# Kernel tuning notes

Hardware: AMD Instinct MI355X
Metric: run time of the kernel (lower is better)

## Reference

```python
import jax, jax.numpy as jnp
import numpy as np

N, D, E, H, K = 4096, 512, 32, 128, 4  # tokens, d_model, n_experts, expert hidden, top-k


def setup_inputs() -> dict:
    key = jax.random.key(0)
    k0, k1, k2, k3 = jax.random.split(key, 4)
    x = jax.random.normal(k0, (N, D), dtype=jnp.float32)
    # router weights, init std = d**-0.5 (matches get_initializer std)
    expert_sel = jax.random.normal(k1, (E, D), dtype=jnp.float32) * (D ** -0.5)
    # per-expert MLP weights (Linear stores [out, in]; we keep [E, in, out] layout)
    w1 = jax.random.normal(k2, (E, D, H), dtype=jnp.float32) * (D ** -0.5)
    w2 = jax.random.normal(k3, (E, H, D), dtype=jnp.float32) * (H ** -0.5)
    return {"x": x, "expert_sel": expert_sel, "w1": w1, "w2": w2}


def reference(x, expert_sel, w1, w2):
    # routing: sigmoid selection, top-k experts per token
    scores = jax.nn.sigmoid(x @ expert_sel.T)          # [N, E]
    gate_vals, gate_idx = jax.lax.top_k(scores, K)     # [N, K]
    # dense gate matrix with only top-k nonzero (sparse dispatch/combine weights)
    gate = (jax.nn.one_hot(gate_idx, E, dtype=x.dtype) * gate_vals[..., None]).sum(-2)  # [N, E]
    # per-expert MLP; gating at hidden is exact since experts have no bias:
    # gate * (relu(x W1) W2) == (gate * relu(x W1)) W2
    h = jax.nn.relu(jnp.einsum('nd,edh->neh', x, w1)) * gate[..., None]  # [N, E, H]
    y = jnp.einsum('neh,ehv->nv', h, w2)               # [N, D]
    return y
```

## Files before the change

### kernel.cpp

```cpp
#include <hip/hip_runtime.h>
#include <hip/hip_bf16.h>

#define NTOK 4096
#define DM   512
#define NE   32
#define HD   128
#define TK   4

typedef unsigned short u16;
typedef unsigned int   u32;
typedef u16   u16x4 __attribute__((ext_vector_type(4)));
typedef u16   u16x8 __attribute__((ext_vector_type(8)));
typedef short short8 __attribute__((ext_vector_type(8)));
typedef float f32x4 __attribute__((ext_vector_type(4)));

__device__ __forceinline__ u16 f2bf(float f) {
    union { float f; u32 u; } v; v.f = f;
    return (u16)((v.u + 0x7FFFu + ((v.u >> 16) & 1u)) >> 16);
}
__device__ __forceinline__ float bf2f(u16 h) {
    union { u32 u; float f; } v; v.u = ((u32)h) << 16; return v.f;
}

__global__ __launch_bounds__(256) void prep_kernel(const float* __restrict__ x,
                                                   const float* __restrict__ sel,
                                                   const float* __restrict__ w1,
                                                   const float* __restrict__ w2,
                                                   int* __restrict__ counts_pad,
                                                   int* __restrict__ tok_list,
                                                   float* __restrict__ gate_list,
                                                   u16* __restrict__ xbf,
                                                   u16* __restrict__ wf1,
                                                   u16* __restrict__ wf2) {
    __shared__ float  xs[4][520];
    __shared__ double sc[4][33];
    int tid = threadIdx.x;
    int wv = tid >> 6, lane = tid & 63;

    if (blockIdx.x >= 1024) {
        int m = lane & 15, q = lane >> 4;
        int f0 = ((blockIdx.x - 1024) * 4 + wv) * 2;
        const float* in[2]; u16* outp[2]; int Nd[2];
#pragma unroll
        for (int u = 0; u < 2; ++u) {
            int w = f0 + u;
            if (w < 4096) {
                int e = w >> 7, rem = w & 127, ks = rem >> 3, nt = rem & 7;
                in[u] = w1 + (size_t)e * DM * HD + (size_t)(32 * ks + q * 8) * HD + 16 * nt + m;
                Nd[u] = HD;
                outp[u] = wf1 + (size_t)w * 512 + lane * 8;
            } else {
                int wl = w - 4096, e = wl >> 7, rem = wl & 127, ks = rem >> 5, nt = rem & 31;
                in[u] = w2 + (size_t)e * HD * DM + (size_t)(32 * ks + q * 8) * DM + 16 * nt + m;
                Nd[u] = DM;
                outp[u] = wf2 + (size_t)wl * 512 + lane * 8;
            }
        }
        float v[2][8];
#pragma unroll
        for (int u = 0; u < 2; ++u)
#pragma unroll
            for (int j = 0; j < 8; ++j) v[u][j] = in[u][(size_t)j * Nd[u]];
#pragma unroll
        for (int u = 0; u < 2; ++u) {
            u16x8 h;
#pragma unroll
            for (int j = 0; j < 8; ++j) h[j] = f2bf(v[u][j]);
            *(u16x8*)outp[u] = h;
        }
        return;
    }

    int tb = blockIdx.x * 4;
#pragma unroll
    for (int rep = 0; rep < 2; ++rep) {
        int idx = (rep * 256 + tid) * 4;
        int row = idx >> 9, col = idx & 511;
        f32x4 v = *(const f32x4*)(x + (size_t)(tb + row) * DM + col);
        *(f32x4*)&xs[row][col] = v;
        u16x4 h;
#pragma unroll
        for (int j = 0; j < 4; ++j) h[j] = f2bf(v[j]);
        *(u16x4*)(xbf + (size_t)(tb + row) * DM + col) = h;
    }
    __syncthreads();

    int tok = tid & 3, seg = (tid >> 2) & 1, e = tid >> 3;
    const float* sp = sel + (size_t)e * DM + seg * 256;
    const float* xp = &xs[tok][seg * 256];
    double pa = 0.0, pb = 0.0, pc = 0.0, pd = 0.0;
#pragma unroll 4
    for (int j = 0; j < 256; j += 16) {
        f32x4 x0 = *(const f32x4*)(xp + j);
        f32x4 x1 = *(const f32x4*)(xp + j + 4);
        f32x4 x2 = *(const f32x4*)(xp + j + 8);
        f32x4 x3 = *(const f32x4*)(xp + j + 12);
        f32x4 s0 = *(const f32x4*)(sp + j);
        f32x4 s1 = *(const f32x4*)(sp + j + 4);
        f32x4 s2 = *(const f32x4*)(sp + j + 8);
        f32x4 s3 = *(const f32x4*)(sp + j + 12);
#pragma unroll
        for (int k = 0; k < 4; ++k) {
            pa = fma((double)x0[k], (double)s0[k], pa);
            pb = fma((double)x1[k], (double)s1[k], pb);
            pc = fma((double)x2[k], (double)s2[k], pc);
            pd = fma((double)x3[k], (double)s3[k], pd);
        }
    }
    double p = (pa + pb) + (pc + pd);
    p += __shfl_xor(p, 4);
    if (seg == 0) sc[tok][e] = p;
    __syncthreads();

    if (tid < 4) {
        int t = tb + tid;
        unsigned mask = 0;
        for (int k = 0; k < TK; ++k) {
            double best = -1e300; int be = 0;
            for (int ee = 0; ee < NE; ++ee) {
                double v = sc[tid][ee];
                if (!((mask >> ee) & 1u) && v > best) { best = v; be = ee; }
            }
            mask |= 1u << be;
            float gate = 1.0f / (1.0f + __expf(-(float)best));
            int pos = atomicAdd(&counts_pad[32 * be], 1);
            tok_list[be * NTOK + pos]  = (k << 16) | t;
            gate_list[be * NTOK + pos] = gate;
        }
    }
}

__global__ __launch_bounds__(256, 2) void moe_mlp_kernel(const u16* __restrict__ xbf,
                                                         const u16* __restrict__ wf1,
                                                         const u16* __restrict__ wf2,
                                                         const int* __restrict__ counts_pad,
                                                         const int* __restrict__ tok_list,
                                                         const float* __restrict__ gate_list,
                                                         u16* __restrict__ part,
                                                         float* __restrict__ out,
                                                         int use_part) {
    __shared__ int   s_cnt[NE];
    __shared__ int   s_ent[32];
    __shared__ float s_gate[32];
    __shared__ __align__(16) u16 Hm[32][136];
    __shared__ __align__(16) u16 Ct[32][520];

    int tid = threadIdx.x;
    if (tid < NE) s_cnt[tid] = counts_pad[32 * tid];
    __syncthreads();

    int b = blockIdx.x;
    int xcd = b & 7, idx = b >> 3;
    int e = -1, t = 0, rows = 0, pre = 0;
#pragma unroll
    for (int j = 0; j < 4; ++j) {
        int ee = xcd + 8 * j;
        int cc = s_cnt[ee];
        int nt = (cc + 31) >> 5;
        if (e < 0 && idx < pre + nt) { e = ee; t = idx - pre; rows = cc - t * 32; if (rows > 32) rows = 32; }
        pre += nt;
    }
    if (e < 0) return;

    if (tid < 32) {
        int base = e * NTOK + t * 32;
        bool val = tid < rows;
        s_ent[tid]  = tok_list[base + (val ? tid : 0)];
        s_gate[tid] = val ? gate_list[base + tid] : 0.0f;
    }
    __syncthreads();

    int wv = tid >> 6, lane = tid & 63, m = lane & 15, q = lane >> 4;
    int r = wv >> 1, c = wv & 1;
    const u16* w1f = wf1 + (size_t)e * (128 * 512);
    const u16* w2f = wf2 + (size_t)e * (128 * 512);

    const u16* a0 = xbf + (size_t)(s_ent[16 * r + m] & 0xFFFF) * DM + q * 8;

    short8 ab[2][2];
    short8 bb[2][2][4];
#pragma unroll
    for (int kk = 0; kk < 2; ++kk) {
        ab[0][kk] = *(const short8*)(a0 + 32 * kk);
        const u16* bp = w1f + (size_t)kk * 4096 + (size_t)(4 * c) * 512 + lane * 8;
#pragma unroll
        for (int n = 0; n < 4; ++n) bb[0][kk][n] = *(const short8*)(bp + n * 512);
    }
    f32x4 acc[4];
#pragma unroll
    for (int n = 0; n < 4; ++n) acc[n] = (f32x4){0.f, 0.f, 0.f, 0.f};

#pragma unroll
    for (int kp = 0; kp < 8; ++kp) {
        int cur = kp & 1, nxt = cur ^ 1;
        if (kp < 7) {
            int ks0 = 2 * (kp + 1);
#pragma unroll
            for (int kk = 0; kk < 2; ++kk) {
                ab[nxt][kk] = *(const short8*)(a0 + 32 * (ks0 + kk));
                const u16* bp = w1f + (size_t)(ks0 + kk) * 4096 + (size_t)(4 * c) * 512 + lane * 8;
#pragma unroll
                for (int n = 0; n < 4; ++n) bb[nxt][kk][n] = *(const short8*)(bp + n * 512);
            }
        }
#pragma unroll
        for (int kk = 0; kk < 2; ++kk)
#pragma unroll
            for (int n = 0; n < 4; ++n)
                acc[n] = __builtin_amdgcn_mfma_f32_16x16x32_bf16(ab[cur][kk],
                                                                 bb[cur][kk][n],
                                                                 acc[n], 0, 0, 0);
    }

    {
        int rb = 16 * r + q * 4;
#pragma unroll
        for (int n = 0; n < 4; ++n)
#pragma unroll
            for (int rr = 0; rr < 4; ++rr)
                Hm[rb + rr][64 * c + 16 * n + m] =
                    f2bf(fmaxf(acc[n][rr], 0.f) * s_gate[rb + rr]);
    }

    short8 cb[2][8];
    {
        const u16* bp = w2f + (size_t)(wv * 8) * 512 + lane * 8;
#pragma unroll
        for (int n = 0; n < 8; ++n) cb[0][n] = *(const short8*)(bp + n * 512);
    }
    __syncthreads();

    f32x4 acc2[2][8];
#pragma unroll
    for (int i = 0; i < 2; ++i)
#pragma unroll
        for (int n = 0; n < 8; ++n) acc2[i][n] = (f32x4){0.f, 0.f, 0.f, 0.f};
#pragma unroll
    for (int ks = 0; ks < 4; ++ks) {
        int cur = ks & 1, nxt = cur ^ 1;
        if (ks < 3) {
            const u16* bp = w2f + (size_t)((ks + 1) * 32 + wv * 8) * 512 + lane * 8;
#pragma unroll
            for (int n = 0; n < 8; ++n) cb[nxt][n] = *(const short8*)(bp + n * 512);
        }
        short8 h0 = *(const short8*)&Hm[m][32 * ks + q * 8];
        short8 h1 = *(const short8*)&Hm[16 + m][32 * ks + q * 8];
#pragma unroll
        for (int n = 0; n < 8; ++n) {
            acc2[0][n] = __builtin_amdgcn_mfma_f32_16x16x32_bf16(h0, cb[cur][n], acc2[0][n], 0, 0, 0);
            acc2[1][n] = __builtin_amdgcn_mfma_f32_16x16x32_bf16(h1, cb[cur][n], acc2[1][n], 0, 0, 0);
        }
    }

#pragma unroll
    for (int i = 0; i < 2; ++i) {
        int rb = 16 * i + q * 4;
#pragma unroll
        for (int n = 0; n < 8; ++n)
#pragma unroll
            for (int rr = 0; rr < 4; ++rr)
                Ct[rb + rr][128 * wv + 16 * n + m] = f2bf(acc2[i][n][rr]);
    }
    __syncthreads();
#pragma unroll
    for (int rep = 0; rep < 8; ++rep) {
        int rl = rep * 4 + wv;
        u16x8 v = *(const u16x8*)&Ct[rl][lane * 8];
        if (rl < rows) {
            int en = s_ent[rl];
            int tk = en & 0xFFFF, sl2 = en >> 16;
            if (use_part) {
                *(u16x8*)(part + ((size_t)sl2 * NTOK + tk) * DM + lane * 8) = v;
            } else {
                float* op = out + (size_t)tk * DM + lane * 8;
#pragma unroll
                for (int j = 0; j < 8; ++j) atomicAdd(&op[j], bf2f(v[j]));
            }
        }
    }
}

__global__ __launch_bounds__(256) void combine_kernel(const u16* __restrict__ part,
                                                      float* __restrict__ out) {
    size_t off = ((size_t)blockIdx.x * 256 + threadIdx.x) * 8;
    float s[8] = {0, 0, 0, 0, 0, 0, 0, 0};
#pragma unroll
    for (int k = 0; k < TK; ++k) {
        u16x8 p = *(const u16x8*)(part + (size_t)k * NTOK * DM + off);
#pragma unroll
        for (int j = 0; j < 8; ++j) s[j] += bf2f(p[j]);
    }
    *(f32x4*)(out + off)     = (f32x4){s[0], s[1], s[2], s[3]};
    *(f32x4*)(out + off + 4) = (f32x4){s[4], s[5], s[6], s[7]};
}

extern "C" void kernel_launch(void* const* d_in, const int* in_sizes, int n_in,
                              void* d_out, int out_size, void* d_ws, size_t ws_size,
                              hipStream_t stream) {
    const float* x   = (const float*)d_in[0];
    const float* sel = (const float*)d_in[1];
    const float* w1  = (const float*)d_in[2];
    const float* w2  = (const float*)d_in[3];
    float* out = (float*)d_out;

    char* ws = (char*)d_ws;
    int*   counts_pad = (int*)(ws);
    int*   tok_list   = (int*)(ws + 4096);
    float* gate_list  = (float*)(ws + 4096 + (size_t)NE * NTOK * 4);
    u16*   xbf  = (u16*)(ws + 4096 + (size_t)NE * NTOK * 8);
    u16*   wf1  = xbf + (size_t)NTOK * DM;
    u16*   wf2  = wf1 + (size_t)NE * HD * DM;
    u16*   part = wf2 + (size_t)NE * HD * DM;

    size_t need = 4096 + (size_t)NE * NTOK * 8 + (size_t)NTOK * DM * 2
                + 2 * (size_t)NE * HD * DM * 2 + (size_t)TK * NTOK * DM * 2;
    int use_part = (ws_size >= need) ? 1 : 0;

    hipMemsetAsync(counts_pad, 0, 4096, stream);
    if (!use_part)
        hipMemsetAsync(d_out, 0, (size_t)NTOK * DM * sizeof(float), stream);

    prep_kernel<<<2048, 256, 0, stream>>>(x, sel, w1, w2, counts_pad, tok_list,
                                          gate_list, xbf, wf1, wf2);
    moe_mlp_kernel<<<4096, 256, 0, stream>>>(xbf, wf1, wf2, counts_pad, tok_list,
                                             gate_list, part, out, use_part);
    if (use_part)
        combine_kernel<<<NTOK * DM / 8 / 256, 256, 0, stream>>>(part, out);
}
```

Measured before the change: 117.7 us.

## Fuse prep, expert MLP and combine into one persistent kernel with grid barriers

```diff
diff --git a/kernel.cpp b/kernel.cpp
--- a/kernel.cpp
+++ b/kernel.cpp
@@ -6,6 +6,7 @@
 #define NE   32
 #define HD   128
 #define TK   4
+#define NBLK 512
 
 typedef unsigned short u16;
 typedef unsigned int   u32;
@@ -20,6 +21,283 @@
 }
 __device__ __forceinline__ float bf2f(u16 h) {
     union { u32 u; float f; } v; v.u = ((u32)h) << 16; return v.f;
+}
+
+__device__ __forceinline__ void grid_sync(u32* bar, u32 target) {
+    __syncthreads();
+    if (threadIdx.x == 0) {
+        __hip_atomic_fetch_add(bar, 1u, __ATOMIC_ACQ_REL, __HIP_MEMORY_SCOPE_AGENT);
+        while (__hip_atomic_load(bar, __ATOMIC_ACQUIRE, __HIP_MEMORY_SCOPE_AGENT) < target)
+            __builtin_amdgcn_s_sleep(2);
+    }
+    __syncthreads();
+}
+
+__global__ __launch_bounds__(256, 2) void fused_moe(
+        const float* __restrict__ x, const float* __restrict__ sel,
+        const float* __restrict__ w1, const float* __restrict__ w2,
+        int* __restrict__ counts_pad, u32* __restrict__ bar,
+        int* __restrict__ tok_list, float* __restrict__ gate_list,
+        u16* __restrict__ xbf, u16* __restrict__ wf1, u16* __restrict__ wf2,
+        u16* __restrict__ part, float* __restrict__ out) {
+    __shared__ __align__(16) float  xs[8][520];
+    __shared__ double sc[8][33];
+    __shared__ int    s_cnt[NE];
+    __shared__ int    s_ent[32];
+    __shared__ float  s_gate[32];
+    __shared__ __align__(16) u16 Hm[32][136];
+    __shared__ __align__(16) u16 Ct[32][520];
+
+    int tid = threadIdx.x;
+    int wv = tid >> 6, lane = tid & 63;
+    int b = blockIdx.x;
+
+    {
+        int m = lane & 15, q = lane >> 4;
+#pragma unroll
+        for (int un = 0; un < 2; ++un) {
+            int bs = b + un * NBLK;
+            int f0 = (bs * 4 + wv) * 2;
+            const float* in[2]; u16* outp[2]; int Nd[2];
+#pragma unroll
+            for (int u = 0; u < 2; ++u) {
+                int w = f0 + u;
+                if (w < 4096) {
+                    int e = w >> 7, rem = w & 127, ks = rem >> 3, nt = rem & 7;
+                    in[u] = w1 + (size_t)e * DM * HD + (size_t)(32 * ks + q * 8) * HD + 16 * nt + m;
+                    Nd[u] = HD;
+                    outp[u] = wf1 + (size_t)w * 512 + lane * 8;
+                } else {
+                    int wl = w - 4096, e = wl >> 7, rem = wl & 127, ks = rem >> 5, nt = rem & 31;
+                    in[u] = w2 + (size_t)e * HD * DM + (size_t)(32 * ks + q * 8) * DM + 16 * nt + m;
+                    Nd[u] = DM;
+                    outp[u] = wf2 + (size_t)wl * 512 + lane * 8;
+                }
+            }
+            float v[2][8];
+#pragma unroll
+            for (int u = 0; u < 2; ++u)
+#pragma unroll
+                for (int j = 0; j < 8; ++j) v[u][j] = in[u][(size_t)j * Nd[u]];
+#pragma unroll
+            for (int u = 0; u < 2; ++u) {
+                u16x8 h;
+#pragma unroll
+                for (int j = 0; j < 8; ++j) h[j] = f2bf(v[u][j]);
+                *(u16x8*)outp[u] = h;
+            }
+        }
+    }
+
+    {
+        int tb = b * 8;
+#pragma unroll
+        for (int rep = 0; rep < 4; ++rep) {
+            int idx = (rep * 256 + tid) * 4;
+            int row = idx >> 9, col = idx & 511;
+            f32x4 v = *(const f32x4*)(x + (size_t)(tb + row) * DM + col);
+            *(f32x4*)&xs[row][col] = v;
+            u16x4 h;
+#pragma unroll
+            for (int j = 0; j < 4; ++j) h[j] = f2bf(v[j]);
+            *(u16x4*)(xbf + (size_t)(tb + row) * DM + col) = h;
+        }
+        __syncthreads();
+
+        int tok = tid & 7, e = tid >> 3;
+        const float* sp = sel + (size_t)e * DM;
+        const float* xp = xs[tok];
+        double pa = 0.0, pb = 0.0, pc = 0.0, pd = 0.0;
+#pragma unroll 4
+        for (int j = 0; j < 512; j += 16) {
+            f32x4 x0 = *(const f32x4*)(xp + j);
+            f32x4 x1 = *(const f32x4*)(xp + j + 4);
+            f32x4 x2 = *(const f32x4*)(xp + j + 8);
+            f32x4 x3 = *(const f32x4*)(xp + j + 12);
+            f32x4 s0 = *(const f32x4*)(sp + j);
+            f32x4 s1 = *(const f32x4*)(sp + j + 4);
+            f32x4 s2 = *(const f32x4*)(sp + j + 8);
+            f32x4 s3 = *(const f32x4*)(sp + j + 12);
+#pragma unroll
+            for (int k = 0; k < 4; ++k) {
+                pa = fma((double)x0[k], (double)s0[k], pa);
+                pb = fma((double)x1[k], (double)s1[k], pb);
+                pc = fma((double)x2[k], (double)s2[k], pc);
+                pd = fma((double)x3[k], (double)s3[k], pd);
+            }
+        }
+        sc[tok][e] = (pa + pb) + (pc + pd);
+        __syncthreads();
+
+        if (tid < 8) {
+            int t = tb + tid;
+            unsigned mask = 0;
+            for (int k = 0; k < TK; ++k) {
+                double best = -1e300; int be = 0;
+                for (int ee = 0; ee < NE; ++ee) {
+                    double v = sc[tid][ee];
+                    if (!((mask >> ee) & 1u) && v > best) { best = v; be = ee; }
+                }
+                mask |= 1u << be;
+                float gate = 1.0f / (1.0f + __expf(-(float)best));
+                int pos = atomicAdd(&counts_pad[32 * be], 1);
+                tok_list[be * NTOK + pos]  = (k << 16) | t;
+                gate_list[be * NTOK + pos] = gate;
+            }
+        }
+    }
+
+    grid_sync(bar, NBLK);
+
+    {
+        if (tid < NE)
+            s_cnt[tid] = __hip_atomic_load(counts_pad + 32 * tid,
+                                           __ATOMIC_RELAXED, __HIP_MEMORY_SCOPE_AGENT);
+        __syncthreads();
+
+        int xcd = b & 7, idx0 = b >> 3;
+        int c0 = s_cnt[xcd], c1 = s_cnt[xcd + 8], c2 = s_cnt[xcd + 16], c3 = s_cnt[xcd + 24];
+        int n0 = (c0 + 31) >> 5, n1 = (c1 + 31) >> 5, n2 = (c2 + 31) >> 5, n3 = (c3 + 31) >> 5;
+        int tot = n0 + n1 + n2 + n3;
+
+        int m = lane & 15, q = lane >> 4;
+        int r = wv >> 1, c = wv & 1;
+
+        for (int idx = idx0; idx < tot; idx += 64) {
+            int e2, t2;
+            if (idx < n0)                { e2 = xcd;      t2 = idx; }
+            else if (idx < n0 + n1)      { e2 = xcd + 8;  t2 = idx - n0; }
+            else if (idx < n0 + n1 + n2) { e2 = xcd + 16; t2 = idx - n0 - n1; }
+            else                         { e2 = xcd + 24; t2 = idx - n0 - n1 - n2; }
+            int cc = s_cnt[e2];
+            int rows = cc - t2 * 32; if (rows > 32) rows = 32;
+
+            __syncthreads();
+            if (tid < 32) {
+                int base = e2 * NTOK + t2 * 32;
+                bool val = tid < rows;
+                s_ent[tid]  = tok_list[base + (val ? tid : 0)];
+                s_gate[tid] = val ? gate_list[base + tid] : 0.0f;
+            }
+            __syncthreads();
+
+            const u16* w1f = wf1 + (size_t)e2 * (128 * 512);
+            const u16* w2f = wf2 + (size_t)e2 * (128 * 512);
+            const u16* a0 = xbf + (size_t)(s_ent[16 * r + m] & 0xFFFF) * DM + q * 8;
+
+            short8 ab[2][2];
+            short8 bb[2][2][4];
+#pragma unroll
+            for (int kk = 0; kk < 2; ++kk) {
+                ab[0][kk] = *(const short8*)(a0 + 32 * kk);
+                const u16* bp = w1f + (size_t)kk * 4096 + (size_t)(4 * c) * 512 + lane * 8;
+#pragma unroll
+                for (int n = 0; n < 4; ++n) bb[0][kk][n] = *(const short8*)(bp + n * 512);
+            }
+            f32x4 acc[4];
+#pragma unroll
+            for (int n = 0; n < 4; ++n) acc[n] = (f32x4){0.f, 0.f, 0.f, 0.f};
+
+#pragma unroll
+            for (int kp = 0; kp < 8; ++kp) {
+                int cur = kp & 1, nxt = cur ^ 1;
+                if (kp < 7) {
+                    int ks0 = 2 * (kp + 1);
+#pragma unroll
+                    for (int kk = 0; kk < 2; ++kk) {
+                        ab[nxt][kk] = *(const short8*)(a0 + 32 * (ks0 + kk));
+                        const u16* bp = w1f + (size_t)(ks0 + kk) * 4096 + (size_t)(4 * c) * 512 + lane * 8;
+#pragma unroll
+                        for (int n = 0; n < 4; ++n) bb[nxt][kk][n] = *(const short8*)(bp + n * 512);
+                    }
+                }
+#pragma unroll
+                for (int kk = 0; kk < 2; ++kk)
+#pragma unroll
+                    for (int n = 0; n < 4; ++n)
+                        acc[n] = __builtin_amdgcn_mfma_f32_16x16x32_bf16(ab[cur][kk],
+                                                                         bb[cur][kk][n],
+                                                                         acc[n], 0, 0, 0);
+            }
+
+            {
+                int rb = 16 * r + q * 4;
+#pragma unroll
+                for (int n = 0; n < 4; ++n)
+#pragma unroll
+                    for (int rr = 0; rr < 4; ++rr)
+                        Hm[rb + rr][64 * c + 16 * n + m] =
+                            f2bf(fmaxf(acc[n][rr], 0.f) * s_gate[rb + rr]);
+            }
+
+            short8 cb[2][8];
+            {
+                const u16* bp = w2f + (size_t)(wv * 8) * 512 + lane * 8;
+#pragma unroll
+                for (int n = 0; n < 8; ++n) cb[0][n] = *(const short8*)(bp + n * 512);
+            }
+            __syncthreads();
+
+            f32x4 acc2[2][8];
+#pragma unroll
+            for (int i = 0; i < 2; ++i)
+#pragma unroll
+                for (int n = 0; n < 8; ++n) acc2[i][n] = (f32x4){0.f, 0.f, 0.f, 0.f};
+#pragma unroll
+            for (int ks = 0; ks < 4; ++ks) {
+                int cur = ks & 1, nxt = cur ^ 1;
+                if (ks < 3) {
+                    const u16* bp = w2f + (size_t)((ks + 1) * 32 + wv * 8) * 512 + lane * 8;
+#pragma unroll
+                    for (int n = 0; n < 8; ++n) cb[nxt][n] = *(const short8*)(bp + n * 512);
+                }
+                short8 h0 = *(const short8*)&Hm[m][32 * ks + q * 8];
+                short8 h1 = *(const short8*)&Hm[16 + m][32 * ks + q * 8];
+#pragma unroll
+                for (int n = 0; n < 8; ++n) {
+                    acc2[0][n] = __builtin_amdgcn_mfma_f32_16x16x32_bf16(h0, cb[cur][n], acc2[0][n], 0, 0, 0);
+                    acc2[1][n] = __builtin_amdgcn_mfma_f32_16x16x32_bf16(h1, cb[cur][n], acc2[1][n], 0, 0, 0);
+                }
+            }
+
+#pragma unroll
+            for (int i = 0; i < 2; ++i) {
+                int rb = 16 * i + q * 4;
+#pragma unroll
+                for (int n = 0; n < 8; ++n)
+#pragma unroll
+                    for (int rr = 0; rr < 4; ++rr)
+                        Ct[rb + rr][128 * wv + 16 * n + m] = f2bf(acc2[i][n][rr]);
+            }
+            __syncthreads();
+#pragma unroll
+            for (int rep = 0; rep < 8; ++rep) {
+                int rl = rep * 4 + wv;
+                u16x8 v = *(const u16x8*)&Ct[rl][lane * 8];
+                if (rl < rows) {
+                    int en = s_ent[rl];
+                    int tk = en & 0xFFFF, sl2 = en >> 16;
+                    *(u16x8*)(part + ((size_t)sl2 * NTOK + tk) * DM + lane * 8) = v;
+                }
+            }
+        }
+    }
+
+    grid_sync(bar, 2u * NBLK);
+
+#pragma unroll
+    for (int rep = 0; rep < 2; ++rep) {
+        size_t off = (((size_t)b + (size_t)rep * NBLK) * 256 + tid) * 8;
+        float s[8] = {0, 0, 0, 0, 0, 0, 0, 0};
+#pragma unroll
+        for (int k = 0; k < TK; ++k) {
+            u16x8 p = *(const u16x8*)(part + (size_t)k * NTOK * DM + off);
+#pragma unroll
+            for (int j = 0; j < 8; ++j) s[j] += bf2f(p[j]);
+        }
+        *(f32x4*)(out + off)     = (f32x4){s[0], s[1], s[2], s[3]};
+        *(f32x4*)(out + off + 4) = (f32x4){s[4], s[5], s[6], s[7]};
+    }
 }
 
 __global__ __launch_bounds__(256) void prep_kernel(const float* __restrict__ x,
@@ -136,9 +414,7 @@
                                                          const int* __restrict__ counts_pad,
                                                          const int* __restrict__ tok_list,
                                                          const float* __restrict__ gate_list,
-                                                         u16* __restrict__ part,
-                                                         float* __restrict__ out,
-                                                         int use_part) {
+                                                         float* __restrict__ out) {
     __shared__ int   s_cnt[NE];
     __shared__ int   s_ent[32];
     __shared__ float s_gate[32];
@@ -174,7 +450,6 @@
     int r = wv >> 1, c = wv & 1;
     const u16* w1f = wf1 + (size_t)e * (128 * 512);
     const u16* w2f = wf2 + (size_t)e * (128 * 512);
-
     const u16* a0 = xbf + (size_t)(s_ent[16 * r + m] & 0xFFFF) * DM + q * 8;
 
     short8 ab[2][2];
@@ -207,8 +482,7 @@
         for (int kk = 0; kk < 2; ++kk)
 #pragma unroll
             for (int n = 0; n < 4; ++n)
-                acc[n] = __builtin_amdgcn_mfma_f32_16x16x32_bf16(ab[cur][kk],
-                                                                 bb[cur][kk][n],
+                acc[n] = __builtin_amdgcn_mfma_f32_16x16x32_bf16(ab[cur][kk], bb[cur][kk][n],
                                                                  acc[n], 0, 0, 0);
     }
 
@@ -218,8 +492,7 @@
         for (int n = 0; n < 4; ++n)
 #pragma unroll
             for (int rr = 0; rr < 4; ++rr)
-                Hm[rb + rr][64 * c + 16 * n + m] =
-                    f2bf(fmaxf(acc[n][rr], 0.f) * s_gate[rb + rr]);
+                Hm[rb + rr][64 * c + 16 * n + m] = f2bf(fmaxf(acc[n][rr], 0.f) * s_gate[rb + rr]);
     }
 
     short8 cb[2][8];
@@ -268,35 +541,18 @@
         u16x8 v = *(const u16x8*)&Ct[rl][lane * 8];
         if (rl < rows) {
             int en = s_ent[rl];
-            int tk = en & 0xFFFF, sl2 = en >> 16;
-            if (use_part) {
-                *(u16x8*)(part + ((size_t)sl2 * NTOK + tk) * DM + lane * 8) = v;
-            } else {
-                float* op = out + (size_t)tk * DM + lane * 8;
-#pragma unroll
-                for (int j = 0; j < 8; ++j) atomicAdd(&op[j], bf2f(v[j]));
-            }
-        }
-    }
-}
-
-__global__ __launch_bounds__(256) void combine_kernel(const u16* __restrict__ part,
-                                                      float* __restrict__ out) {
-    size_t off = ((size_t)blockIdx.x * 256 + threadIdx.x) * 8;
-    float s[8] = {0, 0, 0, 0, 0, 0, 0, 0};
-#pragma unroll
-    for (int k = 0; k < TK; ++k) {
-        u16x8 p = *(const u16x8*)(part + (size_t)k * NTOK * DM + off);
-#pragma unroll
-        for (int j = 0; j < 8; ++j) s[j] += bf2f(p[j]);
-    }
-    *(f32x4*)(out + off)     = (f32x4){s[0], s[1], s[2], s[3]};
-    *(f32x4*)(out + off + 4) = (f32x4){s[4], s[5], s[6], s[7]};
+            int tk = en & 0xFFFF;
+            float* op = out + (size_t)tk * DM + lane * 8;
+#pragma unroll
+            for (int j = 0; j < 8; ++j) atomicAdd(&op[j], bf2f(v[j]));
+        }
+    }
 }
 
 extern "C" void kernel_launch(void* const* d_in, const int* in_sizes, int n_in,
                               void* d_out, int out_size, void* d_ws, size_t ws_size,
                               hipStream_t stream) {
+    (void)in_sizes; (void)n_in; (void)out_size;
     const float* x   = (const float*)d_in[0];
     const float* sel = (const float*)d_in[1];
     const float* w1  = (const float*)d_in[2];
@@ -305,25 +561,28 @@
 
     char* ws = (char*)d_ws;
     int*   counts_pad = (int*)(ws);
-    int*   tok_list   = (int*)(ws + 4096);
-    float* gate_list  = (float*)(ws + 4096 + (size_t)NE * NTOK * 4);
-    u16*   xbf  = (u16*)(ws + 4096 + (size_t)NE * NTOK * 8);
+    u32*   bar        = (u32*)(ws + 4096);
+    int*   tok_list   = (int*)(ws + 4352);
+    float* gate_list  = (float*)(ws + 4352 + (size_t)NE * NTOK * 4);
+    u16*   xbf  = (u16*)(ws + 4352 + (size_t)NE * NTOK * 8);
     u16*   wf1  = xbf + (size_t)NTOK * DM;
     u16*   wf2  = wf1 + (size_t)NE * HD * DM;
     u16*   part = wf2 + (size_t)NE * HD * DM;
 
-    size_t need = 4096 + (size_t)NE * NTOK * 8 + (size_t)NTOK * DM * 2
+    size_t need = 4352 + (size_t)NE * NTOK * 8 + (size_t)NTOK * DM * 2
                 + 2 * (size_t)NE * HD * DM * 2 + (size_t)TK * NTOK * DM * 2;
-    int use_part = (ws_size >= need) ? 1 : 0;
-
-    hipMemsetAsync(counts_pad, 0, 4096, stream);
-    if (!use_part)
+
+    if (ws_size >= need) {
+        hipMemsetAsync(ws, 0, 4352, stream);
+        fused_moe<<<NBLK, 256, 0, stream>>>(x, sel, w1, w2, counts_pad, bar,
+                                            tok_list, gate_list, xbf, wf1, wf2,
+                                            part, out);
+    } else {
+        hipMemsetAsync(counts_pad, 0, 4096, stream);
         hipMemsetAsync(d_out, 0, (size_t)NTOK * DM * sizeof(float), stream);
-
-    prep_kernel<<<2048, 256, 0, stream>>>(x, sel, w1, w2, counts_pad, tok_list,
-                                          gate_list, xbf, wf1, wf2);
-    moe_mlp_kernel<<<4096, 256, 0, stream>>>(xbf, wf1, wf2, counts_pad, tok_list,
-                                             gate_list, part, out, use_part);
-    if (use_part)
-        combine_kernel<<<NTOK * DM / 8 / 256, 256, 0, stream>>>(part, out);
-}
+        prep_kernel<<<2048, 256, 0, stream>>>(x, sel, w1, w2, counts_pad, tok_list,
+                                              gate_list, xbf, wf1, wf2);
+        moe_mlp_kernel<<<4096, 256, 0, stream>>>(xbf, wf1, wf2, counts_pad, tok_list,
+                                                 gate_list, out);
+    }
+}
```

Measured after the change: 246.8 us. +109.7%, slower.

## Route 16 tokens per prep block and batch per-expert atomics

Applied to the files above, without the earlier changes.

```diff
diff --git a/kernel.cpp b/kernel.cpp
--- a/kernel.cpp
+++ b/kernel.cpp
@@ -32,14 +32,16 @@
                                                    u16* __restrict__ xbf,
                                                    u16* __restrict__ wf1,
                                                    u16* __restrict__ wf2) {
-    __shared__ float  xs[4][520];
-    __shared__ double sc[4][33];
+    __shared__ __align__(16) float  xs[16][524];
+    __shared__ double sc[16][33];
+    __shared__ int    pk_e[64];
+    __shared__ float  pk_g[64];
     int tid = threadIdx.x;
     int wv = tid >> 6, lane = tid & 63;
 
-    if (blockIdx.x >= 1024) {
+    if (blockIdx.x >= 256) {
         int m = lane & 15, q = lane >> 4;
-        int f0 = ((blockIdx.x - 1024) * 4 + wv) * 2;
+        int f0 = ((blockIdx.x - 256) * 4 + wv) * 2;
         const float* in[2]; u16* outp[2]; int Nd[2];
 #pragma unroll
         for (int u = 0; u < 2; ++u) {
@@ -71,9 +73,9 @@
         return;
     }
 
-    int tb = blockIdx.x * 4;
-#pragma unroll
-    for (int rep = 0; rep < 2; ++rep) {
+    int tb = blockIdx.x * 16;
+#pragma unroll
+    for (int rep = 0; rep < 8; ++rep) {
         int idx = (rep * 256 + tid) * 4;
         int row = idx >> 9, col = idx & 511;
         f32x4 v = *(const f32x4*)(x + (size_t)(tb + row) * DM + col);
@@ -85,35 +87,45 @@
     }
     __syncthreads();
 
-    int tok = tid & 3, seg = (tid >> 2) & 1, e = tid >> 3;
-    const float* sp = sel + (size_t)e * DM + seg * 256;
-    const float* xp = &xs[tok][seg * 256];
-    double pa = 0.0, pb = 0.0, pc = 0.0, pd = 0.0;
+    {
+        int tok0 = tid & 7, e = tid >> 3;
+        const float* sp  = sel + (size_t)e * DM;
+        const float* xpA = xs[tok0];
+        const float* xpB = xs[tok0 + 8];
+        double a0 = 0.0, a1 = 0.0, a2 = 0.0, a3 = 0.0;
+        double b0 = 0.0, b1 = 0.0, b2 = 0.0, b3 = 0.0;
 #pragma unroll 4
-    for (int j = 0; j < 256; j += 16) {
-        f32x4 x0 = *(const f32x4*)(xp + j);
-        f32x4 x1 = *(const f32x4*)(xp + j + 4);
-        f32x4 x2 = *(const f32x4*)(xp + j + 8);
-        f32x4 x3 = *(const f32x4*)(xp + j + 12);
-        f32x4 s0 = *(const f32x4*)(sp + j);
-        f32x4 s1 = *(const f32x4*)(sp + j + 4);
-        f32x4 s2 = *(const f32x4*)(sp + j + 8);
-        f32x4 s3 = *(const f32x4*)(sp + j + 12);
-#pragma unroll
-        for (int k = 0; k < 4; ++k) {
-            pa = fma((double)x0[k], (double)s0[k], pa);
-            pb = fma((double)x1[k], (double)s1[k], pb);
-            pc = fma((double)x2[k], (double)s2[k], pc);
-            pd = fma((double)x3[k], (double)s3[k], pd);
-        }
-    }
-    double p = (pa + pb) + (pc + pd);
-    p += __shfl_xor(p, 4);
-    if (seg == 0) sc[tok][e] = p;
-    __syncthreads();
-
-    if (tid < 4) {
-        int t = tb + tid;
+        for (int j = 0; j < 512; j += 16) {
+            f32x4 s0 = *(const f32x4*)(sp + j);
+            f32x4 s1 = *(const f32x4*)(sp + j + 4);
+            f32x4 s2 = *(const f32x4*)(sp + j + 8);
+            f32x4 s3 = *(const f32x4*)(sp + j + 12);
+            f32x4 xA0 = *(const f32x4*)(xpA + j);
+            f32x4 xA1 = *(const f32x4*)(xpA + j + 4);
+            f32x4 xA2 = *(const f32x4*)(xpA + j + 8);
+            f32x4 xA3 = *(const f32x4*)(xpA + j + 12);
+            f32x4 xB0 = *(const f32x4*)(xpB + j);
+            f32x4 xB1 = *(const f32x4*)(xpB + j + 4);
+            f32x4 xB2 = *(const f32x4*)(xpB + j + 8);
+            f32x4 xB3 = *(const f32x4*)(xpB + j + 12);
+#pragma unroll
+            for (int k = 0; k < 4; ++k) {
+                a0 = fma((double)xA0[k], (double)s0[k], a0);
+                a1 = fma((double)xA1[k], (double)s1[k], a1);
+                a2 = fma((double)xA2[k], (double)s2[k], a2);
+                a3 = fma((double)xA3[k], (double)s3[k], a3);
+                b0 = fma((double)xB0[k], (double)s0[k], b0);
+                b1 = fma((double)xB1[k], (double)s1[k], b1);
+                b2 = fma((double)xB2[k], (double)s2[k], b2);
+                b3 = fma((double)xB3[k], (double)s3[k], b3);
+            }
+        }
+        sc[tok0][e]     = (a0 + a1) + (a2 + a3);
+        sc[tok0 + 8][e] = (b0 + b1) + (b2 + b3);
+    }
+    __syncthreads();
+
+    if (tid < 16) {
         unsigned mask = 0;
         for (int k = 0; k < TK; ++k) {
             double best = -1e300; int be = 0;
@@ -122,10 +134,26 @@
                 if (!((mask >> ee) & 1u) && v > best) { best = v; be = ee; }
             }
             mask |= 1u << be;
-            float gate = 1.0f / (1.0f + __expf(-(float)best));
-            int pos = atomicAdd(&counts_pad[32 * be], 1);
-            tok_list[be * NTOK + pos]  = (k << 16) | t;
-            gate_list[be * NTOK + pos] = gate;
+            pk_e[tid * 4 + k] = be;
+            pk_g[tid * 4 + k] = 1.0f / (1.0f + __expf(-(float)best));
+        }
+    }
+    __syncthreads();
+
+    if (tid < NE) {
+        int e2 = tid, cnt = 0;
+#pragma unroll
+        for (int i = 0; i < 64; ++i) cnt += (pk_e[i] == e2) ? 1 : 0;
+        if (cnt) {
+            int base = atomicAdd(&counts_pad[32 * e2], cnt);
+            int o = 0;
+            for (int i = 0; i < 64; ++i) {
+                if (pk_e[i] == e2) {
+                    tok_list[e2 * NTOK + base + o]  = ((i & 3) << 16) | (tb + (i >> 2));
+                    gate_list[e2 * NTOK + base + o] = pk_g[i];
+                    ++o;
+                }
+            }
         }
     }
 }
@@ -297,6 +325,7 @@
 extern "C" void kernel_launch(void* const* d_in, const int* in_sizes, int n_in,
                               void* d_out, int out_size, void* d_ws, size_t ws_size,
                               hipStream_t stream) {
+    (void)in_sizes; (void)n_in; (void)out_size;
     const float* x   = (const float*)d_in[0];
     const float* sel = (const float*)d_in[1];
     const float* w1  = (const float*)d_in[2];
@@ -320,7 +349,7 @@
     if (!use_part)
         hipMemsetAsync(d_out, 0, (size_t)NTOK * DM * sizeof(float), stream);
 
-    prep_kernel<<<2048, 256, 0, stream>>>(x, sel, w1, w2, counts_pad, tok_list,
+    prep_kernel<<<1280, 256, 0, stream>>>(x, sel, w1, w2, counts_pad, tok_list,
                                           gate_list, xbf, wf1, wf2);
     moe_mlp_kernel<<<4096, 256, 0, stream>>>(xbf, wf1, wf2, counts_pad, tok_list,
                                              gate_list, part, out, use_part);
```

Measured after the change: 123.2 us. 1.05x slower.

## Replace global atomic expert bucketing with per-block counts and prefix-scan lookup

Applied to the files above, without the earlier changes.

```diff
diff --git a/kernel.cpp b/kernel.cpp
--- a/kernel.cpp
+++ b/kernel.cpp
@@ -6,6 +6,7 @@
 #define NE   32
 #define HD   128
 #define TK   4
+#define NRB  1024
 
 typedef unsigned short u16;
 typedef unsigned int   u32;
@@ -13,6 +14,7 @@
 typedef u16   u16x8 __attribute__((ext_vector_type(8)));
 typedef short short8 __attribute__((ext_vector_type(8)));
 typedef float f32x4 __attribute__((ext_vector_type(4)));
+typedef int   int4v __attribute__((ext_vector_type(4)));
 
 __device__ __forceinline__ u16 f2bf(float f) {
     union { float f; u32 u; } v; v.f = f;
@@ -26,7 +28,7 @@
                                                    const float* __restrict__ sel,
                                                    const float* __restrict__ w1,
                                                    const float* __restrict__ w2,
-                                                   int* __restrict__ counts_pad,
+                                                   int* __restrict__ blk_cnt,
                                                    int* __restrict__ tok_list,
                                                    float* __restrict__ gate_list,
                                                    u16* __restrict__ xbf,
@@ -34,12 +36,14 @@
                                                    u16* __restrict__ wf2) {
     __shared__ float  xs[4][520];
     __shared__ double sc[4][33];
+    __shared__ int    pk_e[16];
+    __shared__ float  pk_g[16];
     int tid = threadIdx.x;
     int wv = tid >> 6, lane = tid & 63;
 
-    if (blockIdx.x >= 1024) {
+    if (blockIdx.x >= NRB) {
         int m = lane & 15, q = lane >> 4;
-        int f0 = ((blockIdx.x - 1024) * 4 + wv) * 2;
+        int f0 = ((blockIdx.x - NRB) * 4 + wv) * 2;
         const float* in[2]; u16* outp[2]; int Nd[2];
 #pragma unroll
         for (int u = 0; u < 2; ++u) {
@@ -71,7 +75,8 @@
         return;
     }
 
-    int tb = blockIdx.x * 4;
+    int bl = blockIdx.x;
+    int tb = bl * 4;
 #pragma unroll
     for (int rep = 0; rep < 2; ++rep) {
         int idx = (rep * 256 + tid) * 4;
@@ -113,7 +118,6 @@
     __syncthreads();
 
     if (tid < 4) {
-        int t = tb + tid;
         unsigned mask = 0;
         for (int k = 0; k < TK; ++k) {
             double best = -1e300; int be = 0;
@@ -122,159 +126,222 @@
                 if (!((mask >> ee) & 1u) && v > best) { best = v; be = ee; }
             }
             mask |= 1u << be;
-            float gate = 1.0f / (1.0f + __expf(-(float)best));
-            int pos = atomicAdd(&counts_pad[32 * be], 1);
-            tok_list[be * NTOK + pos]  = (k << 16) | t;
-            gate_list[be * NTOK + pos] = gate;
-        }
+            pk_e[tid * 4 + k] = be;
+            pk_g[tid * 4 + k] = 1.0f / (1.0f + __expf(-(float)best));
+        }
+    }
+    __syncthreads();
+
+    if (tid < NE) {
+        int e2 = tid, cnt = 0;
+        int base = (e2 * NRB + bl) * 4;
+#pragma unroll
+        for (int i = 0; i < 16; ++i) {
+            if (pk_e[i] == e2) {
+                tok_list[base + cnt]  = ((i & 3) << 16) | (tb + (i >> 2));
+                gate_list[base + cnt] = pk_g[i];
+                ++cnt;
+            }
+        }
+        blk_cnt[e2 * NRB + bl] = cnt;
     }
 }
 
 __global__ __launch_bounds__(256, 2) void moe_mlp_kernel(const u16* __restrict__ xbf,
                                                          const u16* __restrict__ wf1,
                                                          const u16* __restrict__ wf2,
-                                                         const int* __restrict__ counts_pad,
+                                                         const int* __restrict__ blk_cnt,
                                                          const int* __restrict__ tok_list,
                                                          const float* __restrict__ gate_list,
                                                          u16* __restrict__ part,
                                                          float* __restrict__ out,
                                                          int use_part) {
-    __shared__ int   s_cnt[NE];
+    __shared__ int   s_tot[4];
+    __shared__ int   s_red[4][4];
+    __shared__ int   s_pref[NRB + 1];
     __shared__ int   s_ent[32];
     __shared__ float s_gate[32];
     __shared__ __align__(16) u16 Hm[32][136];
     __shared__ __align__(16) u16 Ct[32][520];
 
     int tid = threadIdx.x;
-    if (tid < NE) s_cnt[tid] = counts_pad[32 * tid];
-    __syncthreads();
-
-    int b = blockIdx.x;
-    int xcd = b & 7, idx = b >> 3;
-    int e = -1, t = 0, rows = 0, pre = 0;
+    int wv = tid >> 6, lane = tid & 63;
+    int xcd = blockIdx.x & 7, idx0 = blockIdx.x >> 3;
+
+    int lsums[4];
 #pragma unroll
     for (int j = 0; j < 4; ++j) {
-        int ee = xcd + 8 * j;
-        int cc = s_cnt[ee];
-        int nt = (cc + 31) >> 5;
-        if (e < 0 && idx < pre + nt) { e = ee; t = idx - pre; rows = cc - t * 32; if (rows > 32) rows = 32; }
-        pre += nt;
-    }
-    if (e < 0) return;
-
-    if (tid < 32) {
-        int base = e * NTOK + t * 32;
-        bool val = tid < rows;
-        s_ent[tid]  = tok_list[base + (val ? tid : 0)];
-        s_gate[tid] = val ? gate_list[base + tid] : 0.0f;
-    }
-    __syncthreads();
-
-    int wv = tid >> 6, lane = tid & 63, m = lane & 15, q = lane >> 4;
+        int4v v = *(const int4v*)&blk_cnt[(size_t)(xcd + 8 * j) * NRB + tid * 4];
+        lsums[j] = v[0] + v[1] + v[2] + v[3];
+    }
+#pragma unroll
+    for (int j = 0; j < 4; ++j) {
+        int s = lsums[j];
+#pragma unroll
+        for (int off = 32; off >= 1; off >>= 1) s += __shfl_down(s, off);
+        if (lane == 0) s_red[wv][j] = s;
+    }
+    __syncthreads();
+    if (tid < 4) s_tot[tid] = s_red[0][tid] + s_red[1][tid] + s_red[2][tid] + s_red[3][tid];
+    __syncthreads();
+
+    int c0 = s_tot[0], c1 = s_tot[1], c2 = s_tot[2], c3 = s_tot[3];
+    int n0 = (c0 + 31) >> 5, n1 = (c1 + 31) >> 5, n2 = (c2 + 31) >> 5, n3 = (c3 + 31) >> 5;
+    int tot = n0 + n1 + n2 + n3;
+
+    int m = lane & 15, q = lane >> 4;
     int r = wv >> 1, c = wv & 1;
-    const u16* w1f = wf1 + (size_t)e * (128 * 512);
-    const u16* w2f = wf2 + (size_t)e * (128 * 512);
-
-    const u16* a0 = xbf + (size_t)(s_ent[16 * r + m] & 0xFFFF) * DM + q * 8;
-
-    short8 ab[2][2];
-    short8 bb[2][2][4];
-#pragma unroll
-    for (int kk = 0; kk < 2; ++kk) {
-        ab[0][kk] = *(const short8*)(a0 + 32 * kk);
-        const u16* bp = w1f + (size_t)kk * 4096 + (size_t)(4 * c) * 512 + lane * 8;
-#pragma unroll
-        for (int n = 0; n < 4; ++n) bb[0][kk][n] = *(const short8*)(bp + n * 512);
-    }
-    f32x4 acc[4];
-#pragma unroll
-    for (int n = 0; n < 4; ++n) acc[n] = (f32x4){0.f, 0.f, 0.f, 0.f};
-
-#pragma unroll
-    for (int kp = 0; kp < 8; ++kp) {
-        int cur = kp & 1, nxt = cur ^ 1;
-        if (kp < 7) {
-            int ks0 = 2 * (kp + 1);
-#pragma unroll
-            for (int kk = 0; kk < 2; ++kk) {
-                ab[nxt][kk] = *(const short8*)(a0 + 32 * (ks0 + kk));
-                const u16* bp = w1f + (size_t)(ks0 + kk) * 4096 + (size_t)(4 * c) * 512 + lane * 8;
-#pragma unroll
-                for (int n = 0; n < 4; ++n) bb[nxt][kk][n] = *(const short8*)(bp + n * 512);
-            }
-        }
-#pragma unroll
-        for (int kk = 0; kk < 2; ++kk)
+    int e_last = -1;
+
+    for (int idx = idx0; idx < tot; idx += 128) {
+        int e2, t2, cc;
+        if (idx < n0)                { e2 = xcd;      t2 = idx;                cc = c0; }
+        else if (idx < n0 + n1)      { e2 = xcd + 8;  t2 = idx - n0;           cc = c1; }
+        else if (idx < n0 + n1 + n2) { e2 = xcd + 16; t2 = idx - n0 - n1;      cc = c2; }
+        else                         { e2 = xcd + 24; t2 = idx - n0 - n1 - n2; cc = c3; }
+        int rows = cc - t2 * 32; if (rows > 32) rows = 32;
+
+        __syncthreads();
+
+        if (e2 != e_last) {
+            int4v v = *(const int4v*)&blk_cnt[(size_t)e2 * NRB + tid * 4];
+            int lsum = v[0] + v[1] + v[2] + v[3];
+            int incl = lsum;
+#pragma unroll
+            for (int off = 1; off < 64; off <<= 1) {
+                int t3 = __shfl_up(incl, off);
+                if (lane >= off) incl += t3;
+            }
+            if (lane == 63) s_red[0][wv] = incl;
+            __syncthreads();
+            int woff = 0;
+#pragma unroll
+            for (int w2 = 0; w2 < 4; ++w2) if (w2 < wv) woff += s_red[0][w2];
+            int excl = woff + incl - lsum;
+            s_pref[tid * 4 + 0] = excl;
+            s_pref[tid * 4 + 1] = excl + v[0];
+            s_pref[tid * 4 + 2] = excl + v[0] + v[1];
+            s_pref[tid * 4 + 3] = excl + v[0] + v[1] + v[2];
+            if (tid == 255) s_pref[NRB] = excl + lsum;
+            e_last = e2;
+            __syncthreads();
+        }
+
+        if (tid < 32) {
+            int row = t2 * 32 + tid;
+            bool val = tid < rows;
+            int rr = val ? row : 0;
+            int lo = 0, hi = NRB;
+            while (hi - lo > 1) { int mid = (lo + hi) >> 1; if (s_pref[mid] <= rr) lo = mid; else hi = mid; }
+            int sub = rr - s_pref[lo];
+            s_ent[tid]  = tok_list[((size_t)e2 * NRB + lo) * 4 + sub];
+            s_gate[tid] = val ? gate_list[((size_t)e2 * NRB + lo) * 4 + sub] : 0.0f;
+        }
+        __syncthreads();
+
+        const u16* w1f = wf1 + (size_t)e2 * (128 * 512);
+        const u16* w2f = wf2 + (size_t)e2 * (128 * 512);
+        const u16* a0 = xbf + (size_t)(s_ent[16 * r + m] & 0xFFFF) * DM + q * 8;
+
+        short8 ab[2][2];
+        short8 bb[2][2][4];
+#pragma unroll
+        for (int kk = 0; kk < 2; ++kk) {
+            ab[0][kk] = *(const short8*)(a0 + 32 * kk);
+            const u16* bp = w1f + (size_t)kk * 4096 + (size_t)(4 * c) * 512 + lane * 8;
+#pragma unroll
+            for (int n = 0; n < 4; ++n) bb[0][kk][n] = *(const short8*)(bp + n * 512);
+        }
+        f32x4 acc[4];
+#pragma unroll
+        for (int n = 0; n < 4; ++n) acc[n] = (f32x4){0.f, 0.f, 0.f, 0.f};
+
+#pragma unroll
+        for (int kp = 0; kp < 8; ++kp) {
+            int cur = kp & 1, nxt = cur ^ 1;
+            if (kp < 7) {
+                int ks0 = 2 * (kp + 1);
+#pragma unroll
+                for (int kk = 0; kk < 2; ++kk) {
+                    ab[nxt][kk] = *(const short8*)(a0 + 32 * (ks0 + kk));
+                    const u16* bp = w1f + (size_t)(ks0 + kk) * 4096 + (size_t)(4 * c) * 512 + lane * 8;
+#pragma unroll
+                    for (int n = 0; n < 4; ++n) bb[nxt][kk][n] = *(const short8*)(bp + n * 512);
+                }
+            }
+#pragma unroll
+            for (int kk = 0; kk < 2; ++kk)
+#pragma unroll
+                for (int n = 0; n < 4; ++n)
+                    acc[n] = __builtin_amdgcn_mfma_f32_16x16x32_bf16(ab[cur][kk],
+                                                                     bb[cur][kk][n],
+                                                                     acc[n], 0, 0, 0);
+        }
+
+        {
+            int rb = 16 * r + q * 4;
 #pragma unroll
             for (int n = 0; n < 4; ++n)
-                acc[n] = __builtin_amdgcn_mfma_f32_16x16x32_bf16(ab[cur][kk],
-                                                                 bb[cur][kk][n],
-                                                                 acc[n], 0, 0, 0);
-    }
-
-    {
-        int rb = 16 * r + q * 4;
-#pragma unroll
-        for (int n = 0; n < 4; ++n)
-#pragma unroll
-            for (int rr = 0; rr < 4; ++rr)
-                Hm[rb + rr][64 * c + 16 * n + m] =
-                    f2bf(fmaxf(acc[n][rr], 0.f) * s_gate[rb + rr]);
-    }
-
-    short8 cb[2][8];
-    {
-        const u16* bp = w2f + (size_t)(wv * 8) * 512 + lane * 8;
-#pragma unroll
-        for (int n = 0; n < 8; ++n) cb[0][n] = *(const short8*)(bp + n * 512);
-    }
-    __syncthreads();
-
-    f32x4 acc2[2][8];
-#pragma unroll
-    for (int i = 0; i < 2; ++i)
-#pragma unroll
-        for (int n = 0; n < 8; ++n) acc2[i][n] = (f32x4){0.f, 0.f, 0.f, 0.f};
-#pragma unroll
-    for (int ks = 0; ks < 4; ++ks) {
-        int cur = ks & 1, nxt = cur ^ 1;
-        if (ks < 3) {
-            const u16* bp = w2f + (size_t)((ks + 1) * 32 + wv * 8) * 512 + lane * 8;
-#pragma unroll
-            for (int n = 0; n < 8; ++n) cb[nxt][n] = *(const short8*)(bp + n * 512);
-        }
-        short8 h0 = *(const short8*)&Hm[m][32 * ks + q * 8];
-        short8 h1 = *(const short8*)&Hm[16 + m][32 * ks + q * 8];
-#pragma unroll
-        for (int n = 0; n < 8; ++n) {
-            acc2[0][n] = __builtin_amdgcn_mfma_f32_16x16x32_bf16(h0, cb[cur][n], acc2[0][n], 0, 0, 0);
-            acc2[1][n] = __builtin_amdgcn_mfma_f32_16x16x32_bf16(h1, cb[cur][n], acc2[1][n], 0, 0, 0);
-        }
-    }
-
-#pragma unroll
-    for (int i = 0; i < 2; ++i) {
-        int rb = 16 * i + q * 4;
-#pragma unroll
-        for (int n = 0; n < 8; ++n)
-#pragma unroll
-            for (int rr = 0; rr < 4; ++rr)
-                Ct[rb + rr][128 * wv + 16 * n + m] = f2bf(acc2[i][n][rr]);
-    }
-    __syncthreads();
-#pragma unroll
-    for (int rep = 0; rep < 8; ++rep) {
-        int rl = rep * 4 + wv;
-        u16x8 v = *(const u16x8*)&Ct[rl][lane * 8];
-        if (rl < rows) {
-            int en = s_ent[rl];
-            int tk = en & 0xFFFF, sl2 = en >> 16;
-            if (use_part) {
-                *(u16x8*)(part + ((size_t)sl2 * NTOK + tk) * DM + lane * 8) = v;
-            } else {
-                float* op = out + (size_t)tk * DM + lane * 8;
-#pragma unroll
-                for (int j = 0; j < 8; ++j) atomicAdd(&op[j], bf2f(v[j]));
+#pragma unroll
+                for (int rr2 = 0; rr2 < 4; ++rr2)
+                    Hm[rb + rr2][64 * c + 16 * n + m] =
+                        f2bf(fmaxf(acc[n][rr2], 0.f) * s_gate[rb + rr2]);
+        }
+
+        short8 cb[2][8];
+        {
+            const u16* bp = w2f + (size_t)(wv * 8) * 512 + lane * 8;
+#pragma unroll
+            for (int n = 0; n < 8; ++n) cb[0][n] = *(const short8*)(bp + n * 512);
+        }
+        __syncthreads();
+
+        f32x4 acc2[2][8];
+#pragma unroll
+        for (int i = 0; i < 2; ++i)
+#pragma unroll
+            for (int n = 0; n < 8; ++n) acc2[i][n] = (f32x4){0.f, 0.f, 0.f, 0.f};
+#pragma unroll
+        for (int ks = 0; ks < 4; ++ks) {
+            int cur = ks & 1, nxt = cur ^ 1;
+            if (ks < 3) {
+                const u16* bp = w2f + (size_t)((ks + 1) * 32 + wv * 8) * 512 + lane * 8;
+#pragma unroll
+                for (int n = 0; n < 8; ++n) cb[nxt][n] = *(const short8*)(bp + n * 512);
+            }
+            short8 h0 = *(const short8*)&Hm[m][32 * ks + q * 8];
+            short8 h1 = *(const short8*)&Hm[16 + m][32 * ks + q * 8];
+#pragma unroll
+            for (int n = 0; n < 8; ++n) {
+                acc2[0][n] = __builtin_amdgcn_mfma_f32_16x16x32_bf16(h0, cb[cur][n], acc2[0][n], 0, 0, 0);
+                acc2[1][n] = __builtin_amdgcn_mfma_f32_16x16x32_bf16(h1, cb[cur][n], acc2[1][n], 0, 0, 0);
+            }
+        }
+
+#pragma unroll
+        for (int i = 0; i < 2; ++i) {
+            int rb = 16 * i + q * 4;
+#pragma unroll
+            for (int n = 0; n < 8; ++n)
+#pragma unroll
+                for (int rr2 = 0; rr2 < 4; ++rr2)
+                    Ct[rb + rr2][128 * wv + 16 * n + m] = f2bf(acc2[i][n][rr2]);
+        }
+        __syncthreads();
+#pragma unroll
+        for (int rep = 0; rep < 8; ++rep) {
+            int rl = rep * 4 + wv;
+            u16x8 v = *(const u16x8*)&Ct[rl][lane * 8];
+            if (rl < rows) {
+                int en = s_ent[rl];
+                int tk = en & 0xFFFF, sl2 = en >> 16;
+                if (use_part) {
+                    *(u16x8*)(part + ((size_t)sl2 * NTOK + tk) * DM + lane * 8) = v;
+                } else {
+                    float* op = out + (size_t)tk * DM + lane * 8;
+#pragma unroll
+                    for (int j = 0; j < 8; ++j) atomicAdd(&op[j], bf2f(v[j]));
+                }
             }
         }
     }
@@ -297,6 +364,7 @@
 extern "C" void kernel_launch(void* const* d_in, const int* in_sizes, int n_in,
                               void* d_out, int out_size, void* d_ws, size_t ws_size,
                               hipStream_t stream) {
+    (void)in_sizes; (void)n_in; (void)out_size;
     const float* x   = (const float*)d_in[0];
     const float* sel = (const float*)d_in[1];
     const float* w1  = (const float*)d_in[2];
@@ -304,25 +372,24 @@
     float* out = (float*)d_out;
 
     char* ws = (char*)d_ws;
-    int*   counts_pad = (int*)(ws);
-    int*   tok_list   = (int*)(ws + 4096);
-    float* gate_list  = (float*)(ws + 4096 + (size_t)NE * NTOK * 4);
-    u16*   xbf  = (u16*)(ws + 4096 + (size_t)NE * NTOK * 8);
+    int*   blk_cnt   = (int*)(ws);
+    int*   tok_list  = (int*)(ws + (size_t)NE * NRB * 4);
+    float* gate_list = (float*)(ws + (size_t)NE * NRB * 4 * 5);
+    u16*   xbf  = (u16*)(ws + (size_t)NE * NRB * 4 * 9);
     u16*   wf1  = xbf + (size_t)NTOK * DM;
     u16*   wf2  = wf1 + (size_t)NE * HD * DM;
     u16*   part = wf2 + (size_t)NE * HD * DM;
 
-    size_t need = 4096 + (size_t)NE * NTOK * 8 + (size_t)NTOK * DM * 2
+    size_t need = (size_t)NE * NRB * 4 * 9 + (size_t)NTOK * DM * 2
                 + 2 * (size_t)NE * HD * DM * 2 + (size_t)TK * NTOK * DM * 2;
     int use_part = (ws_size >= need) ? 1 : 0;
 
-    hipMemsetAsync(counts_pad, 0, 4096, stream);
     if (!use_part)
         hipMemsetAsync(d_out, 0, (size_t)NTOK * DM * sizeof(float), stream);
 
-    prep_kernel<<<2048, 256, 0, stream>>>(x, sel, w1, w2, counts_pad, tok_list,
+    prep_kernel<<<2048, 256, 0, stream>>>(x, sel, w1, w2, blk_cnt, tok_list,
                                           gate_list, xbf, wf1, wf2);
-    moe_mlp_kernel<<<4096, 256, 0, stream>>>(xbf, wf1, wf2, counts_pad, tok_list,
+    moe_mlp_kernel<<<1024, 256, 0, stream>>>(xbf, wf1, wf2, blk_cnt, tok_list,
                                              gate_list, part, out, use_part);
     if (use_part)
         combine_kernel<<<NTOK * DM / 8 / 256, 256, 0, stream>>>(part, out);
```

Result: faster. 114.2 us (-3.0%).
